# Performance work log

Measured on AMD Instinct MI355X. Metric: run time of the kernel, lower is better.

Reference implementation:

```python
import jax, jax.numpy as jnp
import numpy as np

B, S, D, H, HD, F = 2, 2048, 2048, 16, 128, 8192
EPS = 1e-5
THETA = 10000.0
NEG = -1e30


def _rmsnorm(x, w):
    v = jnp.mean(jnp.square(x.astype(jnp.float32)), axis=-1, keepdims=True)
    return (x.astype(jnp.float32) * jax.lax.rsqrt(v + EPS)).astype(x.dtype) * w


def _rope(x):
    # x: [B, S, H, HD]; llama-style rotate-half rotary embedding
    inv_freq = 1.0 / (THETA ** (jnp.arange(0, HD, 2, dtype=jnp.float32) / HD))
    ang = jnp.arange(S, dtype=jnp.float32)[:, None] * inv_freq[None, :]  # [S, HD//2]
    cos = jnp.concatenate([jnp.cos(ang), jnp.cos(ang)], axis=-1)[None, :, None, :]
    sin = jnp.concatenate([jnp.sin(ang), jnp.sin(ang)], axis=-1)[None, :, None, :]
    x1, x2 = jnp.split(x, 2, axis=-1)
    return x * cos + jnp.concatenate([-x2, x1], axis=-1) * sin


def _mlp(x, wg, wu, wd):
    # SiLU-gated HiggsAudioMLP: down(silu(gate(x)) * up(x))
    return (jax.nn.silu(x @ wg) * (x @ wu)) @ wd


def setup_inputs() -> dict:
    key = jax.random.key(0)
    ks = jax.random.split(key, 12)
    std = 0.02
    p = lambda k, shape: jax.random.normal(k, shape, dtype=jnp.float32) * std
    return {
        "hidden_states": jax.random.normal(ks[0], (B, S, D), dtype=jnp.float32),
        "audio_out_mask": jax.random.randint(ks[1], (B, S), 0, 2).astype(bool),
        "wq": p(ks[2], (D, H * HD)),
        "wk": p(ks[3], (D, H * HD)),
        "wv": p(ks[4], (D, H * HD)),
        "wo": p(ks[5], (H * HD, D)),
        "input_ln_w": jnp.ones((D,), jnp.float32),
        "post_ln_w": jnp.ones((D,), jnp.float32),
        "audio_post_ln_w": jnp.ones((D,), jnp.float32),
        "w_gate_t": p(ks[6], (D, F)),
        "w_up_t": p(ks[7], (D, F)),
        "w_down_t": p(ks[8], (F, D)),
        "w_gate_a": p(ks[9], (D, F)),
        "w_up_a": p(ks[10], (D, F)),
        "w_down_a": p(ks[11], (F, D)),
    }


def reference(hidden_states, audio_out_mask, wq, wk, wv, wo, input_ln_w, post_ln_w,
              audio_post_ln_w, w_gate_t, w_up_t, w_down_t, w_gate_a, w_up_a, w_down_a):
    # ---- self-attention block ----
    residual = hidden_states
    h = _rmsnorm(hidden_states, input_ln_w)
    q = _rope((h @ wq).reshape(B, S, H, HD))
    k = _rope((h @ wk).reshape(B, S, H, HD))
    v = (h @ wv).reshape(B, S, H, HD)
    scores = jnp.einsum("bqhd,bkhd->bhqk", q, k) / float(np.sqrt(HD))
    causal = jnp.tril(jnp.ones((S, S), bool))
    scores = jnp.where(causal[None, None], scores, NEG)
    attn = jax.nn.softmax(scores, axis=-1)
    ctx = jnp.einsum("bhqk,bkhd->bqhd", attn, v).reshape(B, S, H * HD)
    hidden_states = residual + ctx @ wo
    # ---- dual FFN, per-token routed by audio_out_mask ----
    residual = hidden_states
    text_out = _mlp(_rmsnorm(hidden_states, post_ln_w), w_gate_t, w_up_t, w_down_t)
    audio_out = _mlp(_rmsnorm(hidden_states, audio_post_ln_w), w_gate_a, w_up_a, w_down_a)
    return residual + jnp.where(audio_out_mask[..., None], audio_out, text_out)
```

## Files before the change

kernel.cpp:

```cpp
#include <hip/hip_runtime.h>


#define BB 2
#define SS 2048
#define DD 2048
#define HH 16
#define HDD 128
#define FF 8192
#define TT (BB*SS)
#define RPAD 4608

typedef unsigned short ushort_t;
typedef __bf16 bf16x8 __attribute__((ext_vector_type(8)));
typedef float f32x4 __attribute__((ext_vector_type(4)));

#define DEV static __device__ __forceinline__

DEV float bf2f(ushort_t u) { __bf16 b; __builtin_memcpy(&b, &u, 2); return (float)b; }
DEV ushort_t f2bf(float f) { __bf16 b = (__bf16)f; ushort_t u; __builtin_memcpy(&u, &b, 2); return u; }

DEV void gl_lds16(const ushort_t* g, ushort_t* l) {
    __builtin_amdgcn_global_load_lds((const __attribute__((address_space(1))) void*)g,
                                     (__attribute__((address_space(3))) void*)l, 16, 0, 0);
}

#define BARRIER() do { asm volatile("" ::: "memory"); __builtin_amdgcn_s_barrier(); asm volatile("" ::: "memory"); } while (0)
#define LGKM0()   asm volatile("s_waitcnt lgkmcnt(0)" ::: "memory")

__global__ __launch_bounds__(256) void partition_k(const unsigned char* __restrict__ raw,
                                                   int* __restrict__ perm,
                                                   int* __restrict__ header) {
    __shared__ int flag;
    __shared__ int ct[256], ca[256], st[256], sa[256];
    __shared__ int Nt_s, Na_s;
    const int tid = threadIdx.x;
    if (tid == 0) flag = 0;
    __syncthreads();
    int any = 0;
    for (int i = tid; i < TT; i += 256)
        if ((i & 3) != 0 && raw[i] != 0) any = 1;
    if (any) atomicOr(&flag, 1);
    __syncthreads();
    const int is_byte = flag;
    auto mget = [&](int r) -> int {
        return is_byte ? (raw[r] != 0) : (((const int*)raw)[r] != 0);
    };
    int c0 = 0, c1 = 0;
#pragma unroll
    for (int i = 0; i < 16; ++i) {
        if (mget(tid * 16 + i)) c1++; else c0++;
    }
    ct[tid] = c0; ca[tid] = c1;
    __syncthreads();
    if (tid == 0) {
        int at = 0, aa = 0;
        for (int i = 0; i < 256; ++i) {
            st[i] = at; at += ct[i];
            sa[i] = aa; aa += ca[i];
        }
        Nt_s = at; Na_s = aa;
    }
    __syncthreads();
    const int Nt = Nt_s, Na = Na_s;
    const int A0 = (Nt + 255) & ~255;
    const int live = A0 + ((Na + 255) & ~255);
    int pt = st[tid], pa = A0 + sa[tid];
#pragma unroll
    for (int i = 0; i < 16; ++i) {
        const int r = tid * 16 + i;
        if (mget(r)) perm[pa++] = r; else perm[pt++] = r;
    }
    for (int i = Nt + tid; i < A0; i += 256) perm[i] = -1;
    for (int i = A0 + Na + tid; i < RPAD; i += 256) perm[i] = -1;
    if (tid == 0) { header[0] = Nt; header[1] = A0; header[2] = Na; header[3] = live; }
}

struct ConvSeg { const float* in; ushort_t* out; int K, N, cumEnd; };
struct ConvArgs { ConvSeg s[10]; };

__global__ __launch_bounds__(256) void prep_all(ConvArgs a, int convEnd,
                                                float* __restrict__ cosb,
                                                float* __restrict__ sinb,
                                                const float* __restrict__ hs,
                                                const float* __restrict__ iln,
                                                ushort_t* __restrict__ h_bf) {
    __shared__ float t[32][33];
    const int bid = blockIdx.x;
    const int tid = threadIdx.x;
    if (bid < convEnd) {
        int i = 0;
        while (bid >= a.s[i].cumEnd) ++i;
        const int base = (i == 0) ? 0 : a.s[i - 1].cumEnd;
        const int local = bid - base;
        const float* __restrict__ in = a.s[i].in;
        ushort_t* __restrict__ out = a.s[i].out;
        const int K = a.s[i].K, N = a.s[i].N;
        const int ntile = N >> 5;
        const int n0 = (local % ntile) * 32, k0 = (local / ntile) * 32;
        const int tx = tid & 31, ty = tid >> 5;
#pragma unroll
        for (int j = 0; j < 4; ++j)
            t[ty + 8 * j][tx] = in[(size_t)(k0 + ty + 8 * j) * N + n0 + tx];
        __syncthreads();
#pragma unroll
        for (int j = 0; j < 4; ++j)
            out[(size_t)(n0 + ty + 8 * j) * K + k0 + tx] = f2bf(t[tx][ty + 8 * j]);
    } else if (bid < convEnd + 512) {
        const int idx = (bid - convEnd) * 256 + tid;
        const int s = idx >> 6, i = idx & 63;
        const float inv = powf(10000.0f, -(float)i * (1.0f / 64.0f));
        const float ang = (float)s * inv;
        cosb[idx] = cosf(ang);
        sinb[idx] = sinf(ang);
    } else {
        const int row = bid - convEnd - 512;
        const float4* xr = (const float4*)(hs + (size_t)row * DD);
        float4 v0 = xr[tid * 2], v1 = xr[tid * 2 + 1];
        float ss = v0.x * v0.x + v0.y * v0.y + v0.z * v0.z + v0.w * v0.w
                 + v1.x * v1.x + v1.y * v1.y + v1.z * v1.z + v1.w * v1.w;
#pragma unroll
        for (int d = 1; d < 64; d <<= 1) ss += __shfl_xor(ss, d);
        float* red = &t[0][0];
        if ((tid & 63) == 0) red[tid >> 6] = ss;
        __syncthreads();
        const float tot = red[0] + red[1] + red[2] + red[3];
        const float sc = rsqrtf(tot * (1.0f / DD) + 1e-5f);
        const float4* wr = (const float4*)iln;
        float4 w0 = wr[tid * 2], w1 = wr[tid * 2 + 1];
        ushort_t* o = h_bf + (size_t)row * DD + tid * 8;
        o[0] = f2bf(v0.x * sc * w0.x); o[1] = f2bf(v0.y * sc * w0.y);
        o[2] = f2bf(v0.z * sc * w0.z); o[3] = f2bf(v0.w * sc * w0.w);
        o[4] = f2bf(v1.x * sc * w1.x); o[5] = f2bf(v1.y * sc * w1.y);
        o[6] = f2bf(v1.z * sc * w1.z); o[7] = f2bf(v1.w * sc * w1.w);
    }
}

__global__ __launch_bounds__(256) void rmsnorm_gather(const float* __restrict__ x,
                                                      const float* __restrict__ wt_text,
                                                      const float* __restrict__ wt_audio,
                                                      const int* __restrict__ perm,
                                                      const int* __restrict__ header,
                                                      ushort_t* __restrict__ out) {
    const int i = blockIdx.x, tid = threadIdx.x;
    const int p = perm[i];
    ushort_t* o = out + (size_t)i * DD + tid * 8;
    if (p < 0) {
#pragma unroll
        for (int j = 0; j < 8; ++j) o[j] = 0;
        return;
    }
    const float* wt = (i < header[1]) ? wt_text : wt_audio;
    const float4* xr = (const float4*)(x + (size_t)p * DD);
    float4 v0 = xr[tid * 2], v1 = xr[tid * 2 + 1];
    float ss = v0.x * v0.x + v0.y * v0.y + v0.z * v0.z + v0.w * v0.w
             + v1.x * v1.x + v1.y * v1.y + v1.z * v1.z + v1.w * v1.w;
#pragma unroll
    for (int d = 1; d < 64; d <<= 1) ss += __shfl_xor(ss, d);
    __shared__ float red[4];
    if ((tid & 63) == 0) red[tid >> 6] = ss;
    __syncthreads();
    const float tot = red[0] + red[1] + red[2] + red[3];
    const float sc = rsqrtf(tot * (1.0f / DD) + 1e-5f);
    const float4* wr = (const float4*)wt;
    float4 w0 = wr[tid * 2], w1 = wr[tid * 2 + 1];
    o[0] = f2bf(v0.x * sc * w0.x); o[1] = f2bf(v0.y * sc * w0.y);
    o[2] = f2bf(v0.z * sc * w0.z); o[3] = f2bf(v0.w * sc * w0.w);
    o[4] = f2bf(v1.x * sc * w1.x); o[5] = f2bf(v1.y * sc * w1.y);
    o[6] = f2bf(v1.z * sc * w1.z); o[7] = f2bf(v1.w * sc * w1.w);
}

__global__ __launch_bounds__(256) void rope_qk(ushort_t* __restrict__ qb,
                                               ushort_t* __restrict__ kb,
                                               const float* __restrict__ cosb,
                                               const float* __restrict__ sinb) {
    const int gid = blockIdx.x * 256 + threadIdx.x;
    ushort_t* x = (gid < TT * 1024) ? qb : kb;
    const int g = gid & (TT * 1024 - 1);
    const int row = g >> 10, p = g & 1023;
    const int h = p >> 6, d = p & 63;
    const int s = row & (SS - 1);
    const size_t base = (size_t)row * DD + h * HDD + d;
    const float x1 = bf2f(x[base]), x2 = bf2f(x[base + 64]);
    const float c = cosb[s * 64 + d], sn = sinb[s * 64 + d];
    x[base]      = f2bf(x1 * c - x2 * sn);
    x[base + 64] = f2bf(x2 * c + x1 * sn);
}

template <int EPI>
__global__ __launch_bounds__(512, 2) void gemm_nt8(
    const ushort_t* __restrict__ A, const ushort_t* __restrict__ W,
    int K, ushort_t* __restrict__ o0, ushort_t* __restrict__ o1,
    ushort_t* __restrict__ o2, float* __restrict__ Cf,
    const float* __restrict__ resid) {
    const int nwg = gridDim.x * gridDim.y;
    int bid = blockIdx.y * gridDim.x + blockIdx.x;
    bid = (bid & 7) * (nwg >> 3) + (bid >> 3);
    const int bxx = bid % gridDim.x;
    const int byy = bid / gridDim.x;
    const int m0 = byy * 256;
    int kind = 0, n0;
    const ushort_t* B;
    if (EPI == 0) {
        kind = bxx >> 4;
        n0 = (bxx & 15) * 128;
        B = W + (size_t)kind * DD * DD + (size_t)n0 * K;
    } else {
        n0 = bxx * 128;
        B = W + (size_t)n0 * K;
    }
    __shared__ ushort_t smem[49152];
    const int tid = threadIdx.x;
    const int w = tid >> 6, lane = tid & 63;
    const int wm = w >> 2, wn = w & 3;
    const int f16 = lane & 15, g4 = lane >> 4;
    const int rl = tid >> 3;
    const int cc8 = (((tid & 7) ^ ((tid >> 3) & 7)) * 8);
    const ushort_t* gA = A + (size_t)m0 * K;

    auto stageAq = [&](int buf, int k0, int q) {
        gl_lds16(gA + (size_t)(q * 64 + rl) * K + k0 + cc8,
                 &smem[buf * 24576 + q * 4096 + w * 512]);
    };
    auto stageB2 = [&](int buf, int k0) {
#pragma unroll
        for (int j = 0; j < 2; ++j)
            gl_lds16(B + (size_t)(j * 64 + rl) * K + k0 + cc8,
                     &smem[buf * 24576 + 16384 + j * 4096 + w * 512]);
    };

    const int aBase = (wm * 128 + f16) * 64;
    const int bBase = (wn * 32 + f16) * 64;
    int cswz[2];
    cswz[0] = ((g4 ^ (f16 & 7)) * 8);
    cswz[1] = (((4 + g4) ^ (f16 & 7)) * 8);

    f32x4 acc[8][2] = {};
    bf16x8 af[4][2], bfr[2][2];

    stageAq(0, 0, 0); stageAq(0, 0, 1); stageAq(0, 0, 2); stageAq(0, 0, 3);
    stageB2(0, 0);
    stageAq(1, 64, 0); stageAq(1, 64, 2); stageB2(1, 64);
    asm volatile("s_waitcnt vmcnt(4)" ::: "memory");
    BARRIER();

    const int nt = K / 64;
    for (int t = 0; t < nt; ++t) {
        const int cur = t & 1;
        const int ab = cur * 24576, bb = cur * 24576 + 16384;
#pragma unroll
        for (int m = 0; m < 4; ++m)
#pragma unroll
            for (int ks = 0; ks < 2; ++ks)
                af[m][ks] = *(const bf16x8*)&smem[ab + aBase + m * 1024 + cswz[ks]];
#pragma unroll
        for (int np = 0; np < 2; ++np)
#pragma unroll
            for (int ks = 0; ks < 2; ++ks)
                bfr[np][ks] = *(const bf16x8*)&smem[bb + bBase + np * 1024 + cswz[ks]];
        if (t + 1 < nt) {
            stageAq(1 - cur, (t + 1) * 64, 1);
            stageAq(1 - cur, (t + 1) * 64, 3);
        }
        BARRIER();
        LGKM0();
        __builtin_amdgcn_s_setprio(1);
#pragma unroll
        for (int m = 0; m < 4; ++m)
#pragma unroll
            for (int np = 0; np < 2; ++np)
#pragma unroll
                for (int ks = 0; ks < 2; ++ks)
                    acc[m][np] = __builtin_amdgcn_mfma_f32_16x16x32_bf16(af[m][ks], bfr[np][ks], acc[m][np], 0, 0, 0);
        __builtin_amdgcn_s_setprio(0);
        BARRIER();
#pragma unroll
        for (int m = 0; m < 4; ++m)
#pragma unroll
            for (int ks = 0; ks < 2; ++ks)
                af[m][ks] = *(const bf16x8*)&smem[ab + aBase + (4 + m) * 1024 + cswz[ks]];
        if (t + 2 < nt) {
            stageAq(cur, (t + 2) * 64, 0);
            stageAq(cur, (t + 2) * 64, 2);
            stageB2(cur, (t + 2) * 64);
        }
        BARRIER();
        LGKM0();
        __builtin_amdgcn_s_setprio(1);
#pragma unroll
        for (int m = 0; m < 4; ++m)
#pragma unroll
            for (int np = 0; np < 2; ++np)
#pragma unroll
                for (int ks = 0; ks < 2; ++ks)
                    acc[4 + m][np] = __builtin_amdgcn_mfma_f32_16x16x32_bf16(af[m][ks], bfr[np][ks], acc[4 + m][np], 0, 0, 0);
        __builtin_amdgcn_s_setprio(0);
        if (t + 2 < nt) { asm volatile("s_waitcnt vmcnt(4)" ::: "memory"); }
        else            { asm volatile("s_waitcnt vmcnt(0)" ::: "memory"); }
        BARRIER();
    }

#pragma unroll
    for (int m = 0; m < 8; ++m)
#pragma unroll
        for (int np = 0; np < 2; ++np)
#pragma unroll
            for (int j = 0; j < 4; ++j) {
                const int r = m0 + wm * 128 + m * 16 + g4 * 4 + j;
                const int c = n0 + wn * 32 + np * 16 + f16;
                const float v = acc[m][np][j];
                if (EPI == 0) {
                    const ushort_t vb = f2bf(v);
                    if (kind == 0)      o0[(size_t)r * DD + c] = vb;
                    else if (kind == 1) o1[(size_t)r * DD + c] = vb;
                    else {
                        const int b = r >> 11, s = r & (SS - 1), h = c >> 7, d = c & 127;
                        o2[(((size_t)(b * HH + h) * HDD + d) << 11) + s] = vb;
                    }
                } else {
                    const size_t idx = (size_t)r * DD + c;
                    Cf[idx] = resid[idx] + v;
                }
            }
}

__global__ __launch_bounds__(256, 2) void gemm_down_c(
    const ushort_t* __restrict__ A, const ushort_t* __restrict__ Bt_text,
    const ushort_t* __restrict__ Bt_audio, float* __restrict__ C,
    const int* __restrict__ perm, const int* __restrict__ header) {
    const int m0 = blockIdx.y * 128;
    if (m0 >= header[3]) return;
    const ushort_t* Bt = (m0 >= header[1]) ? Bt_audio : Bt_text;
    __shared__ ushort_t As[128 * 32];
    __shared__ ushort_t Bs[128 * 32];
    const int tid = threadIdx.x;
    const int w = tid >> 6, lane = tid & 63;
    const int n0 = blockIdx.x * 128;
    const int wr = w >> 1, wc = w & 1;
    f32x4 acc[4][4] = {};
    const ushort_t* gA = A + (size_t)m0 * FF;
    const ushort_t* gB = Bt + (size_t)n0 * FF;
    const int c0 = tid, c1 = 256 + tid;
    const int r0 = c0 >> 2, o0 = (c0 & 3) * 8;
    const int r1 = c1 >> 2, o1 = (c1 & 3) * 8;
    ushort_t* lA0 = &As[(w * 64) * 8];
    ushort_t* lA1 = &As[(256 + w * 64) * 8];
    ushort_t* lB0 = &Bs[(w * 64) * 8];
    ushort_t* lB1 = &Bs[(256 + w * 64) * 8];
    for (int k0 = 0; k0 < FF; k0 += 32) {
        __syncthreads();
        gl_lds16(gA + (size_t)r0 * FF + k0 + o0, lA0);
        gl_lds16(gA + (size_t)r1 * FF + k0 + o1, lA1);
        gl_lds16(gB + (size_t)r0 * FF + k0 + o0, lB0);
        gl_lds16(gB + (size_t)r1 * FF + k0 + o1, lB1);
        asm volatile("s_waitcnt vmcnt(0)" ::: "memory");
        __syncthreads();
        const int ko = (lane >> 4) * 8;
        const int ra = wr * 64 + (lane & 15);
        const int rb = wc * 64 + (lane & 15);
        bf16x8 af[4], bfv[4];
#pragma unroll
        for (int mi = 0; mi < 4; ++mi) af[mi] = *(const bf16x8*)&As[(ra + mi * 16) * 32 + ko];
#pragma unroll
        for (int ni = 0; ni < 4; ++ni) bfv[ni] = *(const bf16x8*)&Bs[(rb + ni * 16) * 32 + ko];
#pragma unroll
        for (int mi = 0; mi < 4; ++mi)
#pragma unroll
            for (int ni = 0; ni < 4; ++ni)
                acc[mi][ni] = __builtin_amdgcn_mfma_f32_16x16x32_bf16(af[mi], bfv[ni], acc[mi][ni], 0, 0, 0);
    }
    const int cl = lane & 15, r4 = (lane >> 4) * 4;
#pragma unroll
    for (int mi = 0; mi < 4; ++mi)
#pragma unroll
        for (int ni = 0; ni < 4; ++ni)
#pragma unroll
            for (int j = 0; j < 4; ++j) {
                const int r = m0 + wr * 64 + mi * 16 + r4 + j;
                const int p = perm[r];
                if (p >= 0) {
                    const int c = n0 + wc * 64 + ni * 16 + cl;
                    float* q = C + (size_t)p * DD + c;
                    *q = *q + acc[mi][ni][j];
                }
            }
}

__global__ __launch_bounds__(512, 2) void gemm_gu8(
    const ushort_t* __restrict__ A,
    const ushort_t* __restrict__ Bg_t, const ushort_t* __restrict__ Bu_t,
    const ushort_t* __restrict__ Bg_a, const ushort_t* __restrict__ Bu_a,
    ushort_t* __restrict__ act, const int* __restrict__ header) {
    const int nwg = gridDim.x * gridDim.y;
    int bid = blockIdx.y * gridDim.x + blockIdx.x;
    bid = (bid & 7) * (nwg >> 3) + (bid >> 3);
    const int bx = bid % 64;
    const int by = bid / 64;
    const int m0 = by * 256;
    if (m0 >= header[3]) return;
    const bool audio = (m0 >= header[1]);
    const ushort_t* Bg = audio ? Bg_a : Bg_t;
    const ushort_t* Bu = audio ? Bu_a : Bu_t;
    const int n0g = bx * 128;

    __shared__ ushort_t smem[65536];
    const int tid = threadIdx.x;
    const int w = tid >> 6, lane = tid & 63;
    const int wm = w >> 2, wn = w & 3;
    const int f16 = lane & 15, g4 = lane >> 4;

    const int rl = tid >> 3;
    const int cc8 = (((tid & 7) ^ ((tid >> 3) & 7)) * 8);
    const int wchunk = w * 64;

    const ushort_t* gA = A + (size_t)m0 * DD;

    auto stageA_h = [&](int buf, int k0, int h) {
#pragma unroll
        for (int j = 0; j < 2; ++j) {
            const int r = h * 128 + j * 64 + rl;
            gl_lds16(gA + (size_t)r * DD + k0 + cc8,
                     &smem[buf * 32768 + h * 8192 + (j * 512 + wchunk) * 8]);
        }
    };
    auto stageB_h = [&](int buf, int k0, int h) {
#pragma unroll
        for (int j = 0; j < 2; ++j) {
            const int br = h * 128 + j * 64 + rl;
            const int ty = (br >> 4) & 1;
            const int grow = ((br >> 5) << 4) + (br & 15);
            const ushort_t* src = (ty ? Bu : Bg) + (size_t)(n0g + grow) * DD + k0 + cc8;
            gl_lds16(src, &smem[buf * 32768 + 16384 + h * 8192 + (j * 512 + wchunk) * 8]);
        }
    };

    const int aBase = (wm * 128 + f16) * 64;
    const int bBase = (wn * 64 + f16) * 64;
    int cswz[2];
    cswz[0] = ((g4 ^ (f16 & 7)) * 8);
    cswz[1] = (((4 + g4) ^ (f16 & 7)) * 8);

    f32x4 acc[8][4] = {};
    bf16x8 af[4][2], b0[2][2], b1[2][2];

    stageA_h(0, 0, 0); stageA_h(0, 0, 1);
    stageB_h(0, 0, 0); stageB_h(0, 0, 1);
    stageA_h(1, 64, 0); stageB_h(1, 64, 0);
    asm volatile("s_waitcnt vmcnt(4)" ::: "memory");
    BARRIER();

    const int nt = DD / 64;
    for (int t = 0; t < nt; ++t) {
        const int buf = t & 1, obuf = buf ^ 1;
        const int ab = buf * 32768, bb = buf * 32768 + 16384;
        const int k1 = (t + 1) * 64, k2 = (t + 2) * 64;
        const bool pf1 = (t + 1) < nt, pf2 = (t + 2) < nt;
#pragma unroll
        for (int m = 0; m < 4; ++m)
#pragma unroll
            for (int ks = 0; ks < 2; ++ks)
                af[m][ks] = *(const bf16x8*)&smem[ab + aBase + m * 1024 + cswz[ks]];
#pragma unroll
        for (int n = 0; n < 2; ++n)
#pragma unroll
            for (int ks = 0; ks < 2; ++ks)
                b0[n][ks] = *(const bf16x8*)&smem[bb + bBase + n * 1024 + cswz[ks]];
        if (pf1) stageA_h(obuf, k1, 1);
        BARRIER();
        LGKM0();
        __builtin_amdgcn_s_setprio(1);
#pragma unroll
        for (int m = 0; m < 4; ++m)
#pragma unroll
            for (int n = 0; n < 2; ++n)
#pragma unroll
                for (int ks = 0; ks < 2; ++ks)
                    acc[m][n] = __builtin_amdgcn_mfma_f32_16x16x32_bf16(af[m][ks], b0[n][ks], acc[m][n], 0, 0, 0);
        __builtin_amdgcn_s_setprio(0);
        BARRIER();
#pragma unroll
        for (int n = 0; n < 2; ++n)
#pragma unroll
            for (int ks = 0; ks < 2; ++ks)
                b1[n][ks] = *(const bf16x8*)&smem[bb + bBase + (2 + n) * 1024 + cswz[ks]];
        if (pf1) stageB_h(obuf, k1, 1);
        BARRIER();
        LGKM0();
        __builtin_amdgcn_s_setprio(1);
#pragma unroll
        for (int m = 0; m < 4; ++m)
#pragma unroll
            for (int n = 0; n < 2; ++n)
#pragma unroll
                for (int ks = 0; ks < 2; ++ks)
                    acc[m][2 + n] = __builtin_amdgcn_mfma_f32_16x16x32_bf16(af[m][ks], b1[n][ks], acc[m][2 + n], 0, 0, 0);
        __builtin_amdgcn_s_setprio(0);
        BARRIER();
#pragma unroll
        for (int m = 0; m < 4; ++m)
#pragma unroll
            for (int ks = 0; ks < 2; ++ks)
                af[m][ks] = *(const bf16x8*)&smem[ab + aBase + (4 + m) * 1024 + cswz[ks]];
        if (pf2) stageB_h(buf, k2, 0);
        BARRIER();
        LGKM0();
        __builtin_amdgcn_s_setprio(1);
#pragma unroll
        for (int m = 0; m < 4; ++m)
#pragma unroll
            for (int n = 0; n < 2; ++n)
#pragma unroll
                for (int ks = 0; ks < 2; ++ks)
                    acc[4 + m][n] = __builtin_amdgcn_mfma_f32_16x16x32_bf16(af[m][ks], b0[n][ks], acc[4 + m][n], 0, 0, 0);
        __builtin_amdgcn_s_setprio(0);
        BARRIER();
        if (pf2) stageA_h(buf, k2, 0);
        BARRIER();
        __builtin_amdgcn_s_setprio(1);
#pragma unroll
        for (int m = 0; m < 4; ++m)
#pragma unroll
            for (int n = 0; n < 2; ++n)
#pragma unroll
                for (int ks = 0; ks < 2; ++ks)
                    acc[4 + m][2 + n] = __builtin_amdgcn_mfma_f32_16x16x32_bf16(af[m][ks], b1[n][ks], acc[4 + m][2 + n], 0, 0, 0);
        __builtin_amdgcn_s_setprio(0);
        if (pf2)      { asm volatile("s_waitcnt vmcnt(4)" ::: "memory"); }
        else if (pf1) { asm volatile("s_waitcnt vmcnt(0)" ::: "memory"); }
        BARRIER();
    }

    const int r4 = g4 * 4;
#pragma unroll
    for (int m = 0; m < 8; ++m)
#pragma unroll
        for (int np = 0; np < 2; ++np) {
            const int f = n0g + (wn * 2 + np) * 16 + f16;
#pragma unroll
            for (int j = 0; j < 4; ++j) {
                const int r = m0 + wm * 128 + m * 16 + r4 + j;
                const float g = acc[m][np * 2][j], u = acc[m][np * 2 + 1][j];
                act[(size_t)r * FF + f] = f2bf(g / (1.0f + __expf(-g)) * u);
            }
        }
}

__global__ __launch_bounds__(512, 2) void attn_k(
    const ushort_t* __restrict__ qb, const ushort_t* __restrict__ kb,
    const ushort_t* __restrict__ vt, ushort_t* __restrict__ ctx) {
    __shared__ ushort_t Ks[2][64 * 128];
    __shared__ ushort_t Vs[2][128 * 64];
    __shared__ ushort_t Pw[8][16 * 64];
    const int tid = threadIdx.x, w = tid >> 6, lane = tid & 63;
    const int qt = gridDim.x - 1 - blockIdx.x;
    const int bh = blockIdx.y, b = bh >> 4, h = bh & 15;
    const int q0 = qt * 128 + w * 16;
    const int f16 = lane & 15, g4 = lane >> 4;
    bf16x8 aq[4];
    {
        const ushort_t* qr = qb + ((size_t)(b * SS + q0 + f16)) * DD + h * HDD + g4 * 8;
#pragma unroll
        for (int ko = 0; ko < 4; ++ko) aq[ko] = *(const bf16x8*)(qr + ko * 32);
    }
    auto stageKV = [&](int bufi, int kt) {
        const int sk0 = kt * 64;
#pragma unroll
        for (int i = 0; i < 2; ++i) {
            const int c = i * 512 + tid;
            const int csrc = ((c & 15) ^ ((c >> 4) & 7)) * 8;
            gl_lds16(kb + ((size_t)(b * SS + sk0 + (c >> 4))) * DD + h * HDD + csrc,
                     &Ks[bufi][(i * 512 + w * 64) * 8]);
        }
#pragma unroll
        for (int i = 0; i < 2; ++i) {
            const int c = i * 512 + tid;
            const int csrc = ((c & 7) ^ ((c >> 3) & 7)) * 8;
            gl_lds16(vt + ((size_t)((b * HH + h) * HDD + (c >> 3))) * SS + sk0 + csrc,
                     &Vs[bufi][(i * 512 + w * 64) * 8]);
        }
    };
    f32x4 o[8] = {};
    float mrow[4] = {-3e38f, -3e38f, -3e38f, -3e38f};
    float lrow[4] = {};
    const int nkv = 2 * qt + 2;
    stageKV(0, 0);
    for (int kt = 0; kt < nkv; ++kt) {
        const int cur = kt & 1;
        if (kt < nkv - 1) {
            stageKV(cur ^ 1, kt + 1);
            asm volatile("s_waitcnt vmcnt(4)" ::: "memory");
        } else {
            asm volatile("s_waitcnt vmcnt(0)" ::: "memory");
        }
        BARRIER();
        f32x4 s[4] = {};
#pragma unroll
        for (int ko = 0; ko < 4; ++ko)
#pragma unroll
            for (int ni = 0; ni < 4; ++ni) {
                bf16x8 bk = *(const bf16x8*)&Ks[cur][(ni * 16 + f16) * 128 + (((ko * 4 + g4) ^ (f16 & 7)) * 8)];
                s[ni] = __builtin_amdgcn_mfma_f32_16x16x32_bf16(aq[ko], bk, s[ni], 0, 0, 0);
            }
        const float scale = 0.08838834764831843f;
#pragma unroll
        for (int ni = 0; ni < 4; ++ni)
#pragma unroll
            for (int j = 0; j < 4; ++j) {
                float v = s[ni][j] * scale;
                const int kg = kt * 64 + ni * 16 + f16;
                const int qg = q0 + g4 * 4 + j;
                if (kg > qg) v = -1e30f;
                s[ni][j] = v;
            }
#pragma unroll
        for (int j = 0; j < 4; ++j) {
            float tm = fmaxf(fmaxf(s[0][j], s[1][j]), fmaxf(s[2][j], s[3][j]));
#pragma unroll
            for (int dd = 1; dd < 16; dd <<= 1) tm = fmaxf(tm, __shfl_xor(tm, dd));
            if (!__all(tm <= mrow[j] + 8.0f)) {
                const float mn = fmaxf(mrow[j], tm);
                const float corr = __expf(mrow[j] - mn);
                lrow[j] *= corr;
#pragma unroll
                for (int di = 0; di < 8; ++di) o[di][j] *= corr;
                mrow[j] = mn;
            }
            float sum = 0.f;
#pragma unroll
            for (int ni = 0; ni < 4; ++ni) {
                const float p = __expf(s[ni][j] - mrow[j]);
                s[ni][j] = p;
                sum += p;
            }
#pragma unroll
            for (int dd = 1; dd < 16; dd <<= 1) sum += __shfl_xor(sum, dd);
            lrow[j] += sum;
        }
#pragma unroll
        for (int ni = 0; ni < 4; ++ni)
#pragma unroll
            for (int j = 0; j < 4; ++j) {
                const int prow = g4 * 4 + j;
                const int pcb = ni * 2 + (f16 >> 3);
                Pw[w][prow * 64 + ((pcb ^ (prow & 7)) * 8) + (f16 & 7)] = f2bf(s[ni][j]);
            }
#pragma unroll
        for (int ks = 0; ks < 2; ++ks) {
            bf16x8 pa = *(const bf16x8*)&Pw[w][f16 * 64 + (((ks * 4 + g4) ^ (f16 & 7)) * 8)];
#pragma unroll
            for (int di = 0; di < 8; ++di) {
                bf16x8 bv = *(const bf16x8*)&Vs[cur][(di * 16 + f16) * 64 + (((ks * 4 + g4) ^ (f16 & 7)) * 8)];
                o[di] = __builtin_amdgcn_mfma_f32_16x16x32_bf16(pa, bv, o[di], 0, 0, 0);
            }
        }
        BARRIER();
    }
    float inv[4];
#pragma unroll
    for (int j = 0; j < 4; ++j) inv[j] = 1.0f / lrow[j];
#pragma unroll
    for (int di = 0; di < 8; ++di)
#pragma unroll
        for (int j = 0; j < 4; ++j) {
            const int r = q0 + g4 * 4 + j;
            ctx[((size_t)(b * SS + r)) * DD + h * HDD + di * 16 + f16] = f2bf(o[di][j] * inv[j]);
        }
}

extern "C" void kernel_launch(void* const* d_in, const int* in_sizes, int n_in,
                              void* d_out, int out_size, void* d_ws, size_t ws_size,
                              hipStream_t stream) {
    (void)in_sizes; (void)n_in; (void)out_size; (void)ws_size;
    const float* hs  = (const float*)d_in[0];
    const unsigned char* mask_raw = (const unsigned char*)d_in[1];
    const float* wq  = (const float*)d_in[2];
    const float* wk  = (const float*)d_in[3];
    const float* wv  = (const float*)d_in[4];
    const float* wo  = (const float*)d_in[5];
    const float* iln = (const float*)d_in[6];
    const float* pln = (const float*)d_in[7];
    const float* aln = (const float*)d_in[8];
    const float* wgt = (const float*)d_in[9];
    const float* wut = (const float*)d_in[10];
    const float* wdt = (const float*)d_in[11];
    const float* wga = (const float*)d_in[12];
    const float* wua = (const float*)d_in[13];
    const float* wda = (const float*)d_in[14];

    const size_t SZ_W1 = (size_t)DD * DD * 2;
    const size_t SZ_W2 = (size_t)DD * FF * 2;
    const size_t SZ_A  = (size_t)TT * DD * 2;

    char* ws = (char*)d_ws;
    size_t off = 0;
    auto take = [&](size_t n) { char* p = ws + off; off += n; return p; };
    ushort_t* wq_t  = (ushort_t*)take(SZ_W1);
    ushort_t* wk_t  = (ushort_t*)take(SZ_W1);
    ushort_t* wv_t  = (ushort_t*)take(SZ_W1);
    ushort_t* wo_t  = (ushort_t*)take(SZ_W1);
    ushort_t* wg_tb = (ushort_t*)take(SZ_W2);
    ushort_t* wu_tb = (ushort_t*)take(SZ_W2);
    ushort_t* wd_tb = (ushort_t*)take(SZ_W2);
    ushort_t* wg_ab = (ushort_t*)take(SZ_W2);
    ushort_t* wu_ab = (ushort_t*)take(SZ_W2);
    ushort_t* wd_ab = (ushort_t*)take(SZ_W2);
    char* actreg = take(6 * SZ_A);
    float* cosb = (float*)take((size_t)SS * 64 * 4);
    float* sinb = (float*)take((size_t)SS * 64 * 4);
    int* perm   = (int*)take(RPAD * 4);
    int* header = (int*)take(64);

    ushort_t* h_bf = (ushort_t*)(actreg);
    ushort_t* qb   = (ushort_t*)(actreg + 1 * SZ_A);
    ushort_t* kb   = (ushort_t*)(actreg + 2 * SZ_A);
    ushort_t* vt   = (ushort_t*)(actreg + 3 * SZ_A);
    ushort_t* ctx  = (ushort_t*)(actreg + 4 * SZ_A);
    ushort_t* hn_c  = (ushort_t*)(actreg);
    ushort_t* act_c = (ushort_t*)(actreg + (size_t)RPAD * DD * 2);

    const dim3 blk(256);

    partition_k<<<1, blk, 0, stream>>>(mask_raw, perm, header);

    ConvArgs ca;
    int cum = 0;
    auto seg = [&](int i, const float* in, ushort_t* out, int K, int N) {
        cum += (N / 32) * (K / 32);
        ca.s[i] = ConvSeg{in, out, K, N, cum};
    };
    seg(0, wq, wq_t, DD, DD);
    seg(1, wk, wk_t, DD, DD);
    seg(2, wv, wv_t, DD, DD);
    seg(3, wo, wo_t, DD, DD);
    seg(4, wgt, wg_tb, DD, FF);
    seg(5, wut, wu_tb, DD, FF);
    seg(6, wdt, wd_tb, FF, DD);
    seg(7, wga, wg_ab, DD, FF);
    seg(8, wua, wu_ab, DD, FF);
    seg(9, wda, wd_ab, FF, DD);
    prep_all<<<cum + 512 + TT, blk, 0, stream>>>(ca, cum, cosb, sinb, hs, iln, h_bf);

    gemm_nt8<0><<<dim3(48, TT / 256), dim3(512), 0, stream>>>(
        h_bf, wq_t, DD, qb, kb, vt, nullptr, nullptr);
    rope_qk<<<(2 * TT * 1024) / 256, blk, 0, stream>>>(qb, kb, cosb, sinb);
    attn_k<<<dim3(SS / 128, BB * HH), dim3(512), 0, stream>>>(qb, kb, vt, ctx);
    gemm_nt8<1><<<dim3(DD / 128, TT / 256), dim3(512), 0, stream>>>(
        ctx, wo_t, DD, nullptr, nullptr, nullptr, (float*)d_out, hs);

    rmsnorm_gather<<<RPAD, blk, 0, stream>>>((const float*)d_out, pln, aln, perm, header, hn_c);
    gemm_gu8<<<dim3(FF / 128, RPAD / 256), dim3(512), 0, stream>>>(hn_c, wg_tb, wu_tb, wg_ab, wu_ab, act_c, header);
    gemm_down_c<<<dim3(DD / 128, RPAD / 128), blk, 0, stream>>>(act_c, wd_tb, wd_ab, (float*)d_out, perm, header);
}
```

Baseline: 1.096 ms.

## Fuse RoPE into QKV GEMM epilogue and partition into prep kernel

Applies rotary embedding inside the QKV GEMM epilogue by staging the bf16 tile in shared memory so each element can read its rotate-half partner, which removes the separate rope_qk pass over Q and K. Packs cos/sin into one float2 table. Moves the mask-partition kernel into an extra block of prep_all, saving a launch. The cost is an added shared-memory round trip and barriers in the GEMM epilogue, and RoPE is now applied to bf16-rounded partner values.

After: 1.061 ms. 1.03x faster.

```diff
diff --git a/kernel.cpp b/kernel.cpp
--- a/kernel.cpp
+++ b/kernel.cpp
@@ -27,63 +27,17 @@
 #define BARRIER() do { asm volatile("" ::: "memory"); __builtin_amdgcn_s_barrier(); asm volatile("" ::: "memory"); } while (0)
 #define LGKM0()   asm volatile("s_waitcnt lgkmcnt(0)" ::: "memory")
 
-__global__ __launch_bounds__(256) void partition_k(const unsigned char* __restrict__ raw,
-                                                   int* __restrict__ perm,
-                                                   int* __restrict__ header) {
-    __shared__ int flag;
-    __shared__ int ct[256], ca[256], st[256], sa[256];
-    __shared__ int Nt_s, Na_s;
-    const int tid = threadIdx.x;
-    if (tid == 0) flag = 0;
-    __syncthreads();
-    int any = 0;
-    for (int i = tid; i < TT; i += 256)
-        if ((i & 3) != 0 && raw[i] != 0) any = 1;
-    if (any) atomicOr(&flag, 1);
-    __syncthreads();
-    const int is_byte = flag;
-    auto mget = [&](int r) -> int {
-        return is_byte ? (raw[r] != 0) : (((const int*)raw)[r] != 0);
-    };
-    int c0 = 0, c1 = 0;
-#pragma unroll
-    for (int i = 0; i < 16; ++i) {
-        if (mget(tid * 16 + i)) c1++; else c0++;
-    }
-    ct[tid] = c0; ca[tid] = c1;
-    __syncthreads();
-    if (tid == 0) {
-        int at = 0, aa = 0;
-        for (int i = 0; i < 256; ++i) {
-            st[i] = at; at += ct[i];
-            sa[i] = aa; aa += ca[i];
-        }
-        Nt_s = at; Na_s = aa;
-    }
-    __syncthreads();
-    const int Nt = Nt_s, Na = Na_s;
-    const int A0 = (Nt + 255) & ~255;
-    const int live = A0 + ((Na + 255) & ~255);
-    int pt = st[tid], pa = A0 + sa[tid];
-#pragma unroll
-    for (int i = 0; i < 16; ++i) {
-        const int r = tid * 16 + i;
-        if (mget(r)) perm[pa++] = r; else perm[pt++] = r;
-    }
-    for (int i = Nt + tid; i < A0; i += 256) perm[i] = -1;
-    for (int i = A0 + Na + tid; i < RPAD; i += 256) perm[i] = -1;
-    if (tid == 0) { header[0] = Nt; header[1] = A0; header[2] = Na; header[3] = live; }
-}
-
 struct ConvSeg { const float* in; ushort_t* out; int K, N, cumEnd; };
 struct ConvArgs { ConvSeg s[10]; };
 
 __global__ __launch_bounds__(256) void prep_all(ConvArgs a, int convEnd,
-                                                float* __restrict__ cosb,
-                                                float* __restrict__ sinb,
+                                                float2* __restrict__ cstab,
                                                 const float* __restrict__ hs,
                                                 const float* __restrict__ iln,
-                                                ushort_t* __restrict__ h_bf) {
+                                                ushort_t* __restrict__ h_bf,
+                                                const unsigned char* __restrict__ raw,
+                                                int* __restrict__ perm,
+                                                int* __restrict__ header) {
     __shared__ float t[32][33];
     const int bid = blockIdx.x;
     const int tid = threadIdx.x;
@@ -110,9 +64,8 @@
         const int s = idx >> 6, i = idx & 63;
         const float inv = powf(10000.0f, -(float)i * (1.0f / 64.0f));
         const float ang = (float)s * inv;
-        cosb[idx] = cosf(ang);
-        sinb[idx] = sinf(ang);
-    } else {
+        cstab[idx] = make_float2(cosf(ang), sinf(ang));
+    } else if (bid < convEnd + 512 + TT) {
         const int row = bid - convEnd - 512;
         const float4* xr = (const float4*)(hs + (size_t)row * DD);
         float4 v0 = xr[tid * 2], v1 = xr[tid * 2 + 1];
@@ -132,6 +85,52 @@
         o[2] = f2bf(v0.z * sc * w0.z); o[3] = f2bf(v0.w * sc * w0.w);
         o[4] = f2bf(v1.x * sc * w1.x); o[5] = f2bf(v1.y * sc * w1.y);
         o[6] = f2bf(v1.z * sc * w1.z); o[7] = f2bf(v1.w * sc * w1.w);
+    } else {
+        int* ip = (int*)&t[0][0];
+        int* ct = ip;
+        int* ca = ip + 256;
+        int* st = ip + 512;
+        int* sa = ip + 768;
+        int* misc = ip + 1024;
+        if (tid == 0) misc[0] = 0;
+        __syncthreads();
+        int any = 0;
+        for (int i = tid; i < TT; i += 256)
+            if ((i & 3) != 0 && raw[i] != 0) any = 1;
+        if (any) atomicOr(&misc[0], 1);
+        __syncthreads();
+        const int is_byte = misc[0];
+        auto mget = [&](int r) -> int {
+            return is_byte ? (raw[r] != 0) : (((const int*)raw)[r] != 0);
+        };
+        int c0 = 0, c1 = 0;
+#pragma unroll
+        for (int i = 0; i < 16; ++i) {
+            if (mget(tid * 16 + i)) c1++; else c0++;
+        }
+        ct[tid] = c0; ca[tid] = c1;
+        __syncthreads();
+        if (tid == 0) {
+            int at = 0, aa = 0;
+            for (int i = 0; i < 256; ++i) {
+                st[i] = at; at += ct[i];
+                sa[i] = aa; aa += ca[i];
+            }
+            misc[1] = at; misc[2] = aa;
+        }
+        __syncthreads();
+        const int Nt = misc[1], Na = misc[2];
+        const int A0 = (Nt + 255) & ~255;
+        const int live = A0 + ((Na + 255) & ~255);
+        int pt = st[tid], pa = A0 + sa[tid];
+#pragma unroll
+        for (int i = 0; i < 16; ++i) {
+            const int r = tid * 16 + i;
+            if (mget(r)) perm[pa++] = r; else perm[pt++] = r;
+        }
+        for (int i = Nt + tid; i < A0; i += 256) perm[i] = -1;
+        for (int i = A0 + Na + tid; i < RPAD; i += 256) perm[i] = -1;
+        if (tid == 0) { header[0] = Nt; header[1] = A0; header[2] = Na; header[3] = live; }
     }
 }
 
@@ -169,29 +168,12 @@
     o[6] = f2bf(v1.z * sc * w1.z); o[7] = f2bf(v1.w * sc * w1.w);
 }
 
-__global__ __launch_bounds__(256) void rope_qk(ushort_t* __restrict__ qb,
-                                               ushort_t* __restrict__ kb,
-                                               const float* __restrict__ cosb,
-                                               const float* __restrict__ sinb) {
-    const int gid = blockIdx.x * 256 + threadIdx.x;
-    ushort_t* x = (gid < TT * 1024) ? qb : kb;
-    const int g = gid & (TT * 1024 - 1);
-    const int row = g >> 10, p = g & 1023;
-    const int h = p >> 6, d = p & 63;
-    const int s = row & (SS - 1);
-    const size_t base = (size_t)row * DD + h * HDD + d;
-    const float x1 = bf2f(x[base]), x2 = bf2f(x[base + 64]);
-    const float c = cosb[s * 64 + d], sn = sinb[s * 64 + d];
-    x[base]      = f2bf(x1 * c - x2 * sn);
-    x[base + 64] = f2bf(x2 * c + x1 * sn);
-}
-
 template <int EPI>
 __global__ __launch_bounds__(512, 2) void gemm_nt8(
     const ushort_t* __restrict__ A, const ushort_t* __restrict__ W,
     int K, ushort_t* __restrict__ o0, ushort_t* __restrict__ o1,
     ushort_t* __restrict__ o2, float* __restrict__ Cf,
-    const float* __restrict__ resid) {
+    const float* __restrict__ resid, const float2* __restrict__ cstab) {
     const int nwg = gridDim.x * gridDim.y;
     int bid = blockIdx.y * gridDim.x + blockIdx.x;
     bid = (bid & 7) * (nwg >> 3) + (bid >> 3);
@@ -299,28 +281,55 @@
         BARRIER();
     }
 
-#pragma unroll
-    for (int m = 0; m < 8; ++m)
-#pragma unroll
-        for (int np = 0; np < 2; ++np)
+    if (EPI == 0 && kind <= 1) {
+        ushort_t* outp = (kind == 0) ? o0 : o1;
+        __syncthreads();
+#pragma unroll
+        for (int m = 0; m < 8; ++m)
+#pragma unroll
+            for (int np = 0; np < 2; ++np)
+#pragma unroll
+                for (int j = 0; j < 4; ++j)
+                    smem[(wm * 128 + m * 16 + g4 * 4 + j) * 128 + wn * 32 + np * 16 + f16]
+                        = f2bf(acc[m][np][j]);
+        __syncthreads();
+#pragma unroll
+        for (int m = 0; m < 8; ++m)
 #pragma unroll
             for (int j = 0; j < 4; ++j) {
-                const int r = m0 + wm * 128 + m * 16 + g4 * 4 + j;
-                const int c = n0 + wn * 32 + np * 16 + f16;
-                const float v = acc[m][np][j];
-                if (EPI == 0) {
-                    const ushort_t vb = f2bf(v);
-                    if (kind == 0)      o0[(size_t)r * DD + c] = vb;
-                    else if (kind == 1) o1[(size_t)r * DD + c] = vb;
-                    else {
+                const int rloc = wm * 128 + m * 16 + g4 * 4 + j;
+                const int r = m0 + rloc;
+                const int s = r & (SS - 1);
+#pragma unroll
+                for (int np = 0; np < 2; ++np) {
+                    const int d = wn * 32 + np * 16 + f16;
+                    const float2 cs = cstab[s * 64 + (d & 63)];
+                    const float v = acc[m][np][j];
+                    const float p = bf2f(smem[rloc * 128 + (d ^ 64)]);
+                    const float out = (d < 64) ? (v * cs.x - p * cs.y)
+                                               : (v * cs.x + p * cs.y);
+                    outp[(size_t)r * DD + n0 + d] = f2bf(out);
+                }
+            }
+    } else {
+#pragma unroll
+        for (int m = 0; m < 8; ++m)
+#pragma unroll
+            for (int np = 0; np < 2; ++np)
+#pragma unroll
+                for (int j = 0; j < 4; ++j) {
+                    const int r = m0 + wm * 128 + m * 16 + g4 * 4 + j;
+                    const int c = n0 + wn * 32 + np * 16 + f16;
+                    const float v = acc[m][np][j];
+                    if (EPI == 0) {
                         const int b = r >> 11, s = r & (SS - 1), h = c >> 7, d = c & 127;
-                        o2[(((size_t)(b * HH + h) * HDD + d) << 11) + s] = vb;
+                        o2[(((size_t)(b * HH + h) * HDD + d) << 11) + s] = f2bf(v);
+                    } else {
+                        const size_t idx = (size_t)r * DD + c;
+                        Cf[idx] = resid[idx] + v;
                     }
-                } else {
-                    const size_t idx = (size_t)r * DD + c;
-                    Cf[idx] = resid[idx] + v;
                 }
-            }
+    }
 }
 
 __global__ __launch_bounds__(256, 2) void gemm_down_c(
@@ -704,8 +713,7 @@
     ushort_t* wu_ab = (ushort_t*)take(SZ_W2);
     ushort_t* wd_ab = (ushort_t*)take(SZ_W2);
     char* actreg = take(6 * SZ_A);
-    float* cosb = (float*)take((size_t)SS * 64 * 4);
-    float* sinb = (float*)take((size_t)SS * 64 * 4);
+    float2* cstab = (float2*)take((size_t)SS * 64 * 8);
     int* perm   = (int*)take(RPAD * 4);
     int* header = (int*)take(64);
 
@@ -718,8 +726,6 @@
     ushort_t* act_c = (ushort_t*)(actreg + (size_t)RPAD * DD * 2);
 
     const dim3 blk(256);
-
-    partition_k<<<1, blk, 0, stream>>>(mask_raw, perm, header);
 
     ConvArgs ca;
     int cum = 0;
@@ -737,14 +743,14 @@
     seg(7, wga, wg_ab, DD, FF);
     seg(8, wua, wu_ab, DD, FF);
     seg(9, wda, wd_ab, FF, DD);
-    prep_all<<<cum + 512 + TT, blk, 0, stream>>>(ca, cum, cosb, sinb, hs, iln, h_bf);
+    prep_all<<<cum + 512 + TT + 1, blk, 0, stream>>>(ca, cum, cstab, hs, iln, h_bf,
+                                                     mask_raw, perm, header);
 
     gemm_nt8<0><<<dim3(48, TT / 256), dim3(512), 0, stream>>>(
-        h_bf, wq_t, DD, qb, kb, vt, nullptr, nullptr);
-    rope_qk<<<(2 * TT * 1024) / 256, blk, 0, stream>>>(qb, kb, cosb, sinb);
+        h_bf, wq_t, DD, qb, kb, vt, nullptr, nullptr, cstab);
     attn_k<<<dim3(SS / 128, BB * HH), dim3(512), 0, stream>>>(qb, kb, vt, ctx);
     gemm_nt8<1><<<dim3(DD / 128, TT / 256), dim3(512), 0, stream>>>(
-        ctx, wo_t, DD, nullptr, nullptr, nullptr, (float*)d_out, hs);
+        ctx, wo_t, DD, nullptr, nullptr, nullptr, (float*)d_out, hs, nullptr);
 
     rmsnorm_gather<<<RPAD, blk, 0, stream>>>((const float*)d_out, pln, aln, perm, header, hn_c);
     gemm_gu8<<<dim3(FF / 128, RPAD / 256), dim3(512), 0, stream>>>(hn_c, wg_tb, wu_tb, wg_ab, wu_ab, act_c, header);
```
